# Kernel tuning notes

Hardware: AMD Instinct MI355X
Metric: run time of the kernel (lower is better)

## Reference

```python
import jax, jax.numpy as jnp
import numpy as np

B, S, H, A, I = 64, 512, 1024, 1024, 1024


def setup_inputs() -> dict:
    key = jax.random.key(0)
    ks = jax.random.split(key, 12)
    s = lambda fan_in: 1.0 / np.sqrt(fan_in)
    return {
        "encoded": jax.random.normal(ks[0], (B, S, H), jnp.float32),
        "inputs": jax.random.normal(ks[1], (B, I), jnp.float32),
        "states": jax.random.normal(ks[2], (B, H), jnp.float32),
        # attention params
        "W_enc": jax.random.uniform(ks[3], (H, A), jnp.float32, -s(H), s(H)),
        "b_enc": jnp.zeros((A,), jnp.float32),
        "W_dec": jax.random.uniform(ks[4], (H, A), jnp.float32, -s(H), s(H)),
        "b_dec": jnp.zeros((A,), jnp.float32),
        "w_out": jax.random.uniform(ks[5], (A, 1), jnp.float32, -s(A), s(A)),
        "b_out": jnp.zeros((1,), jnp.float32),
        # GRU cell params (input size = I + H)
        "W_ih": jax.random.uniform(ks[6], (3 * H, I + H), jnp.float32, -s(H), s(H)),
        "W_hh": jax.random.uniform(ks[7], (3 * H, H), jnp.float32, -s(H), s(H)),
        "b_ih": jax.random.uniform(ks[8], (3 * H,), jnp.float32, -s(H), s(H)),
        "b_hh": jax.random.uniform(ks[9], (3 * H,), jnp.float32, -s(H), s(H)),
    }


def reference(encoded, inputs, states, W_enc, b_enc, W_dec, b_dec, w_out, b_out,
              W_ih, W_hh, b_ih, b_hh):
    # setup_memory: project encoder states  [B,S,H] @ [H,A] -> [B,S,A]
    enc_proj = jnp.einsum("bsh,ha->bsa", encoded, W_enc) + b_enc
    # project decoder state and broadcast over S
    dec_proj = states @ W_dec + b_dec                      # [B,A]
    projected = enc_proj + dec_proj[:, None, :]            # [B,S,A]
    scores = jnp.tanh(projected) @ w_out + b_out           # [B,S,1]
    weights = jax.nn.softmax(scores, axis=1)               # [B,S,1]
    attention = jnp.sum(encoded * weights, axis=1)         # [B,H]
    # GRU cell on concatenated input
    x = jnp.concatenate([inputs, attention], axis=1)       # [B,I+H]
    gi = x @ W_ih.T + b_ih                                 # [B,3H]
    gh = states @ W_hh.T + b_hh                            # [B,3H]
    i_r, i_z, i_n = jnp.split(gi, 3, axis=1)
    h_r, h_z, h_n = jnp.split(gh, 3, axis=1)
    r = jax.nn.sigmoid(i_r + h_r)
    z = jax.nn.sigmoid(i_z + h_z)
    n = jnp.tanh(i_n + r * h_n)
    return (1.0 - z) * n + z * states                      # [B,H]
```

## Files before the change

### kernel.cpp

```cpp
#include <hip/hip_runtime.h>
#include <stdint.h>

typedef __bf16 bf16x8 __attribute__((ext_vector_type(8)));
typedef float f32x4 __attribute__((ext_vector_type(4)));
typedef unsigned short u16x8 __attribute__((ext_vector_type(8)));

#define LOG2E 1.4426950408889634f
#define LSTR 32

__device__ __forceinline__ unsigned short f2bf(float f) {
  unsigned int x = __builtin_bit_cast(unsigned int, f);
  x += 0x7FFFu + ((x >> 16) & 1u);
  return (unsigned short)(x >> 16);
}
__device__ __forceinline__ float bflo(unsigned int u) {
  return __builtin_bit_cast(float, u << 16);
}
__device__ __forceinline__ float bfhi(unsigned int u) {
  return __builtin_bit_cast(float, u & 0xffff0000u);
}
__device__ __forceinline__ float tanh_fast(float x) {
  float cx = fminf(fmaxf(x, -15.f), 15.f);
  float e = __builtin_amdgcn_exp2f(cx * (2.f * LOG2E));
  return (e - 1.f) * __builtin_amdgcn_rcpf(e + 1.f);
}
__device__ __forceinline__ float sigmoid_fast(float x) {
  float cx = fminf(fmaxf(x, -30.f), 30.f);
  float e = __builtin_amdgcn_exp2f(cx * LOG2E);
  return e * __builtin_amdgcn_rcpf(e + 1.f);
}
__device__ __forceinline__ ushort4 cvt4(const float4 f) {
  return make_ushort4(f2bf(f.x), f2bf(f.y), f2bf(f.z), f2bf(f.w));
}

__device__ __forceinline__ void gl_lds16(const unsigned short* g,
                                         const unsigned short* lds_base) {
  __builtin_amdgcn_global_load_lds(
      (const __attribute__((address_space(1))) unsigned int*)(uintptr_t)g,
      (__attribute__((address_space(3))) unsigned int*)(unsigned int)(uintptr_t)lds_base,
      16, 0, 0);
}

__global__ __launch_bounds__(256) void k_conv(const float* __restrict__ enc,
                                              unsigned short* __restrict__ encb) {
  const size_t base = ((size_t)blockIdx.x * 256) * 64 + (size_t)threadIdx.x * 8;
  float4 v[16];
#pragma unroll
  for (int c = 0; c < 8; ++c) {
    const size_t i = base + (size_t)c * 2048;
    v[2 * c]     = *(const float4*)(enc + i);
    v[2 * c + 1] = *(const float4*)(enc + i + 4);
  }
#pragma unroll
  for (int c = 0; c < 8; ++c) {
    const size_t i = base + (size_t)c * 2048;
    const ushort4 a = cvt4(v[2 * c]);
    const ushort4 b = cvt4(v[2 * c + 1]);
    u16x8 pk = {a.x, a.y, a.z, a.w, b.x, b.y, b.z, b.w};
    *(u16x8*)(encb + i) = pk;
  }
}

__global__ __launch_bounds__(256) void k_small(
    const float* __restrict__ W_enc, unsigned short* __restrict__ Wt,
    const float* __restrict__ states, const float* __restrict__ W_dec,
    const float* __restrict__ b_dec, const float* __restrict__ b_enc,
    float* __restrict__ dvec, float4* __restrict__ zbase) {
  __shared__ unsigned short tile[64][65];
  __shared__ float red[256];
  const int bid = blockIdx.x;
  const int tid = threadIdx.x;
  if (bid < 256) {
    const int bx = bid & 15, by = bid >> 4;
    const int x = tid & 63, y0 = tid >> 6;
#pragma unroll
    for (int i = y0; i < 64; i += 4)
      tile[i][x] = f2bf(W_enc[(size_t)(by * 64 + i) * 1024 + bx * 64 + x]);
    __syncthreads();
#pragma unroll
    for (int i = y0; i < 64; i += 4)
      Wt[(size_t)(bx * 64 + i) * 1024 + by * 64 + x] = tile[x][i];
  } else if (bid < 768) {
    const int bb = bid - 256;
    const int b = bb >> 3;
    const int a0 = (bb & 7) * 128;
    const int a = tid & 127, half = tid >> 7;
    const float* sp = states + (size_t)b * 1024;
    const float* wp = W_dec + a0 + a;
    float acc = 0.f;
    const int kb = half * 512;
#pragma unroll 8
    for (int k = kb; k < kb + 512; ++k)
      acc += sp[k] * wp[(size_t)k * 1024];
    red[tid] = acc;
    __syncthreads();
    if (tid < 128) {
      float v = red[tid] + red[tid + 128];
      dvec[(size_t)b * 1024 + a0 + tid] = v + b_dec[a0 + tid] + b_enc[a0 + tid];
    }
  } else {
    const float4 z = {0.f, 0.f, 0.f, 0.f};
    zbase[(size_t)(bid - 768) * 256 + tid] = z;
  }
}

__global__ __launch_bounds__(256, 3) void k_scores_bf16(
    const unsigned short* __restrict__ encb,
    const unsigned short* __restrict__ Wt,
    const float* __restrict__ dvec,
    const float* __restrict__ w_out,
    float* __restrict__ scores) {
  __shared__ alignas(16) unsigned short lds[2][8192];
  __shared__ float sc[128];

  const int tid = threadIdx.x;
  const int wave = tid >> 6, lane = tid & 63;
  const int l15 = lane & 15, quad = lane >> 4;
  const int mt = blockIdx.x >> 3;
  const int nt = blockIdx.x & 7;
  const int row0 = mt * 128;
  const int b = row0 >> 9;
  const int wm = (wave >> 1) * 64, wn = (wave & 1) * 64;
  const int srow = lane >> 2;
  const int fsw = ((lane >> 2) & 3) ^ ((lane >> 4) & 3);
  const int skoff = (((lane & 3) ^ fsw) * 8);
  const int rchunk = ((quad ^ ((l15 & 3) ^ ((l15 >> 2) & 3))) * 8);

  if (tid < 128) sc[tid] = 0.f;

  const unsigned short* gsrc[4];
#pragma unroll
  for (int s = 0; s < 4; ++s) {
    const int g = wave * 4 + s;
    gsrc[s] = (g < 8)
        ? encb + (size_t)(row0 + g * 16 + srow) * 1024 + skoff
        : Wt + (size_t)(nt * 128 + (g - 8) * 16 + srow) * 1024 + skoff;
  }

  const f32x4 vz = {0.f, 0.f, 0.f, 0.f};
  f32x4 acc[4][4];
#pragma unroll
  for (int i = 0; i < 4; ++i)
#pragma unroll
    for (int j = 0; j < 4; ++j) acc[i][j] = vz;

#define STAGE(BUF, KK)                                              \
  do {                                                              \
    _Pragma("unroll") for (int s = 0; s < 4; ++s)                   \
        gl_lds16(gsrc[s] + (KK), &lds[BUF][(wave * 4 + s) * 512]);  \
  } while (0)

#define COMPUTE(BUF)                                                          \
  do {                                                                        \
    bf16x8 af[4], bg[4];                                                      \
    _Pragma("unroll") for (int i = 0; i < 4; ++i)                             \
        af[i] = *(const bf16x8*)(&lds[BUF][(wm + i * 16 + l15) * LSTR + rchunk]); \
    _Pragma("unroll") for (int j = 0; j < 4; ++j)                             \
        bg[j] = *(const bf16x8*)(&lds[BUF][4096 + (wn + j * 16 + l15) * LSTR + rchunk]); \
    _Pragma("unroll") for (int i = 0; i < 4; ++i)                             \
      _Pragma("unroll") for (int j = 0; j < 4; ++j)                           \
          acc[i][j] = __builtin_amdgcn_mfma_f32_16x16x32_bf16(af[i], bg[j],   \
                                                              acc[i][j], 0, 0, 0); \
  } while (0)

  STAGE(0, 0);
  __syncthreads();

#pragma unroll 1
  for (int k0 = 0; k0 < 1024; k0 += 64) {
    STAGE(1, k0 + 32);
    COMPUTE(0);
    __syncthreads();
    if (k0 + 64 < 1024) { STAGE(0, k0 + 64); }
    COMPUTE(1);
    __syncthreads();
  }
#undef STAGE
#undef COMPUTE

  float p[4][4];
#pragma unroll
  for (int i = 0; i < 4; ++i)
#pragma unroll
    for (int r = 0; r < 4; ++r) p[i][r] = 0.f;
#pragma unroll
  for (int j = 0; j < 4; ++j) {
    const int a = nt * 128 + wn + j * 16 + l15;
    const float dv = dvec[(size_t)b * 1024 + a];
    const float wo = w_out[a];
#pragma unroll
    for (int i = 0; i < 4; ++i)
#pragma unroll
      for (int r = 0; r < 4; ++r)
        p[i][r] += tanh_fast(acc[i][j][r] + dv) * wo;
  }
#pragma unroll
  for (int i = 0; i < 4; ++i)
#pragma unroll
    for (int r = 0; r < 4; ++r) {
      float v = p[i][r];
      v += __shfl_xor(v, 1);
      v += __shfl_xor(v, 2);
      v += __shfl_xor(v, 4);
      v += __shfl_xor(v, 8);
      if (l15 == 0) atomicAdd(&sc[wm + i * 16 + quad * 4 + r], v);
    }
  __syncthreads();
  if (tid < 128)
    atomicAdd(&scores[(size_t)b * 512 + (row0 & 511) + tid], sc[tid]);
}

__global__ __launch_bounds__(256) void k_scores_f32(
    const float* __restrict__ enc, const unsigned short* __restrict__ Wt,
    const float* __restrict__ dvec, const float* __restrict__ w_out,
    float* __restrict__ scores) {
  __shared__ alignas(16) unsigned short lA[128 * LSTR];
  __shared__ alignas(16) unsigned short lB[128 * LSTR];
  __shared__ float sc[128];
  const int tid = threadIdx.x;
  const int wave = tid >> 6, lane = tid & 63;
  const int l15 = lane & 15, quad = lane >> 4;
  const int mt = blockIdx.x >> 2, nh = blockIdx.x & 3;
  const int row0 = mt * 128, b = row0 >> 9;
  const int wm = (wave >> 1) * 64, wn = (wave & 1) * 64;
  const int srow = lane >> 2, skoff = (lane & 3) * 8;
  if (tid < 128) sc[tid] = 0.f;
  const f32x4 vz = {0.f, 0.f, 0.f, 0.f};
#pragma unroll 1
  for (int t2 = 0; t2 < 2; ++t2) {
    const int nt = nh * 2 + t2;
    f32x4 acc[4][4];
#pragma unroll
    for (int i = 0; i < 4; ++i)
#pragma unroll
      for (int j = 0; j < 4; ++j) acc[i][j] = vz;
#pragma unroll 1
    for (int k0 = 0; k0 < 1024; k0 += 32) {
      ushort4 sa[2][2];
      uint4 vb[2];
#pragma unroll
      for (int rr = 0; rr < 2; ++rr) {
        const int r = wave * 2 + rr;
        const float* ap = enc + (size_t)(row0 + r * 16 + srow) * 1024 + k0 + skoff;
        sa[rr][0] = cvt4(*(const float4*)ap);
        sa[rr][1] = cvt4(*(const float4*)(ap + 4));
        vb[rr] = *(const uint4*)(Wt + (size_t)(nt * 128 + r * 16 + srow) * 1024 + k0 + skoff);
      }
      __syncthreads();
#pragma unroll
      for (int rr = 0; rr < 2; ++rr) {
        const int r = wave * 2 + rr;
        *(ushort4*)(lA + (r * 16 + srow) * LSTR + skoff) = sa[rr][0];
        *(ushort4*)(lA + (r * 16 + srow) * LSTR + skoff + 4) = sa[rr][1];
        *(uint4*)(lB + (r * 16 + srow) * LSTR + skoff) = vb[rr];
      }
      __syncthreads();
      bf16x8 af[4], bg[4];
#pragma unroll
      for (int i = 0; i < 4; ++i)
        af[i] = *(const bf16x8*)(lA + (wm + i * 16 + l15) * LSTR + quad * 8);
#pragma unroll
      for (int j = 0; j < 4; ++j)
        bg[j] = *(const bf16x8*)(lB + (wn + j * 16 + l15) * LSTR + quad * 8);
#pragma unroll
      for (int i = 0; i < 4; ++i)
#pragma unroll
        for (int j = 0; j < 4; ++j)
          acc[i][j] = __builtin_amdgcn_mfma_f32_16x16x32_bf16(af[i], bg[j],
                                                              acc[i][j], 0, 0, 0);
    }
    float p[4][4];
#pragma unroll
    for (int i = 0; i < 4; ++i)
#pragma unroll
      for (int r = 0; r < 4; ++r) p[i][r] = 0.f;
#pragma unroll
    for (int j = 0; j < 4; ++j) {
      const int a = nt * 128 + wn + j * 16 + l15;
      const float dv = dvec[(size_t)b * 1024 + a];
      const float wo = w_out[a];
#pragma unroll
      for (int i = 0; i < 4; ++i)
#pragma unroll
        for (int r = 0; r < 4; ++r)
          p[i][r] += tanh_fast(acc[i][j][r] + dv) * wo;
    }
#pragma unroll
    for (int i = 0; i < 4; ++i)
#pragma unroll
      for (int r = 0; r < 4; ++r) {
        float v = p[i][r];
        v += __shfl_xor(v, 1);
        v += __shfl_xor(v, 2);
        v += __shfl_xor(v, 4);
        v += __shfl_xor(v, 8);
        if (l15 == 0) atomicAdd(&sc[wm + i * 16 + quad * 4 + r], v);
      }
  }
  __syncthreads();
  if (tid < 128)
    atomicAdd(&scores[(size_t)b * 512 + (row0 & 511) + tid], sc[tid]);
}

template <bool ABF16>
__global__ __launch_bounds__(256) void k_attn(const void* __restrict__ encv,
                                              const float* __restrict__ scores,
                                              float* __restrict__ att) {
  const int b = blockIdx.x >> 2;
  const int scn = blockIdx.x & 3;
  const int tid = threadIdx.x;
  __shared__ float w[512];
  __shared__ float redm[4], reds[4];

  const float s0 = scores[(size_t)b * 512 + tid];
  const float s1 = scores[(size_t)b * 512 + 256 + tid];
  float m = fmaxf(s0, s1);
#pragma unroll
  for (int off = 32; off; off >>= 1) m = fmaxf(m, __shfl_xor(m, off));
  const int wv = tid >> 6;
  if ((tid & 63) == 0) redm[wv] = m;
  __syncthreads();
  m = fmaxf(fmaxf(redm[0], redm[1]), fmaxf(redm[2], redm[3]));
  const float e0 = __builtin_amdgcn_exp2f((s0 - m) * LOG2E);
  const float e1 = __builtin_amdgcn_exp2f((s1 - m) * LOG2E);
  float sum = e0 + e1;
#pragma unroll
  for (int off = 32; off; off >>= 1) sum += __shfl_xor(sum, off);
  if ((tid & 63) == 0) reds[wv] = sum;
  __syncthreads();
  sum = reds[0] + reds[1] + reds[2] + reds[3];
  const float inv = 1.f / sum;
  w[tid] = e0 * inv;
  w[tid + 256] = e1 * inv;
  __syncthreads();

  const int h0 = (tid & 127) * 8;
  const int sh = tid >> 7;
  float a[8];
#pragma unroll
  for (int i = 0; i < 8; ++i) a[i] = 0.f;
  const size_t base = ((size_t)(b * 512 + scn * 128 + sh)) * 1024 + h0;
#pragma unroll 4
  for (int i = 0; i < 64; ++i) {
    const float ws_ = w[scn * 128 + sh + 2 * i];
    if constexpr (ABF16) {
      const uint4 v = *(const uint4*)((const unsigned short*)encv + base + (size_t)(2 * i) * 1024);
      a[0] += ws_ * bflo(v.x); a[1] += ws_ * bfhi(v.x);
      a[2] += ws_ * bflo(v.y); a[3] += ws_ * bfhi(v.y);
      a[4] += ws_ * bflo(v.z); a[5] += ws_ * bfhi(v.z);
      a[6] += ws_ * bflo(v.w); a[7] += ws_ * bfhi(v.w);
    } else {
      const float* ep = (const float*)encv + base + (size_t)(2 * i) * 1024;
      const float4 v0 = *(const float4*)ep;
      const float4 v1 = *(const float4*)(ep + 4);
      a[0] += ws_ * v0.x; a[1] += ws_ * v0.y;
      a[2] += ws_ * v0.z; a[3] += ws_ * v0.w;
      a[4] += ws_ * v1.x; a[5] += ws_ * v1.y;
      a[6] += ws_ * v1.z; a[7] += ws_ * v1.w;
    }
  }
#pragma unroll
  for (int i = 0; i < 8; ++i)
    atomicAdd(&att[(size_t)b * 1024 + h0 + i], a[i]);
}

__global__ __launch_bounds__(256) void k_gru_gemm(
    const float* __restrict__ xin,
    const float* __restrict__ att,
    const float* __restrict__ states,
    const float* __restrict__ W_ih,
    const float* __restrict__ W_hh,
    float* __restrict__ gbuf) {
  const int tid = threadIdx.x;
  const int wave = tid >> 6, lane = tid & 63;
  const int l15 = lane & 15, quad = lane >> 4;
  const int kk = blockIdx.x & 3;
  const int rest = blockIdx.x >> 2;
  const bool is_gh = rest >= 48;
  const int nt = is_gh ? rest - 48 : rest;
  const int n0 = nt * 64;
  const int KT = is_gh ? 1024 : 2048;
  const int Kh = KT >> 2;
  const int kbase = kk * Kh;
  const float* W = is_gh ? W_hh : W_ih;
  float* outp = gbuf + (is_gh ? (size_t)64 * 3072 : 0);

  __shared__ alignas(16) unsigned short lA[64 * LSTR];
  __shared__ alignas(16) unsigned short lB[64 * LSTR];

  const f32x4 vz = {0.f, 0.f, 0.f, 0.f};
  f32x4 acc[2][2];
  acc[0][0] = vz; acc[0][1] = vz; acc[1][0] = vz; acc[1][1] = vz;

  const int arow = tid >> 2;
  const int achunk = (tid & 3) * 8;
  const int fswG = ((tid >> 2) & 3) ^ ((tid >> 4) & 3);
  const int wchunk = (((tid & 3) ^ fswG) * 8);
  const int rchunkG = ((quad ^ ((l15 & 3) ^ ((l15 >> 2) & 3))) * 8);
  const int wm2 = (wave >> 1) * 32, wn2 = (wave & 1) * 32;

  float4 ra0, ra1, rb0, rb1;
  auto LOADK = [&](int kg0) {
    const int kg = kg0 + achunk;
    const float* ap = is_gh ? (states + (size_t)arow * 1024 + kg)
                    : (kg < 1024 ? (xin + (size_t)arow * 1024 + kg)
                                 : (att + (size_t)arow * 1024 + (kg - 1024)));
    ra0 = *(const float4*)ap;
    ra1 = *(const float4*)(ap + 4);
    const float* wp = W + (size_t)(n0 + arow) * KT + kg;
    rb0 = *(const float4*)wp;
    rb1 = *(const float4*)(wp + 4);
  };
  LOADK(kbase);

#pragma unroll 1
  for (int k0 = 0; k0 < Kh; k0 += 32) {
    __syncthreads();
    *(ushort4*)(lA + arow * LSTR + wchunk) = cvt4(ra0);
    *(ushort4*)(lA + arow * LSTR + wchunk + 4) = cvt4(ra1);
    *(ushort4*)(lB + arow * LSTR + wchunk) = cvt4(rb0);
    *(ushort4*)(lB + arow * LSTR + wchunk + 4) = cvt4(rb1);
    __syncthreads();
    if (k0 + 32 < Kh) LOADK(kbase + k0 + 32);
    bf16x8 af[2], bg[2];
#pragma unroll
    for (int i = 0; i < 2; ++i)
      af[i] = *(const bf16x8*)(lA + (wm2 + i * 16 + l15) * LSTR + rchunkG);
#pragma unroll
    for (int j = 0; j < 2; ++j)
      bg[j] = *(const bf16x8*)(lB + (wn2 + j * 16 + l15) * LSTR + rchunkG);
#pragma unroll
    for (int i = 0; i < 2; ++i)
#pragma unroll
      for (int j = 0; j < 2; ++j)
        acc[i][j] = __builtin_amdgcn_mfma_f32_16x16x32_bf16(af[i], bg[j],
                                                            acc[i][j], 0, 0, 0);
  }
#pragma unroll
  for (int i = 0; i < 2; ++i)
#pragma unroll
    for (int j = 0; j < 2; ++j)
#pragma unroll
      for (int r = 0; r < 4; ++r) {
        const int m = wm2 + i * 16 + quad * 4 + r;
        const int n = n0 + wn2 + j * 16 + l15;
        atomicAdd(&outp[(size_t)m * 3072 + n], acc[i][j][r]);
      }
}

__global__ void k_gate(const float* __restrict__ gbuf,
                       const float* __restrict__ states,
                       const float* __restrict__ b_ih,
                       const float* __restrict__ b_hh,
                       float* __restrict__ outp) {
  const int idx = blockIdx.x * 256 + threadIdx.x;
  const int b = idx >> 10, h = idx & 1023;
  const float* gi = gbuf + (size_t)b * 3072;
  const float* gh = gbuf + (size_t)64 * 3072 + (size_t)b * 3072;
  const float ir = gi[h] + b_ih[h];
  const float iz = gi[1024 + h] + b_ih[1024 + h];
  const float in_ = gi[2048 + h] + b_ih[2048 + h];
  const float hr = gh[h] + b_hh[h];
  const float hz = gh[1024 + h] + b_hh[1024 + h];
  const float hn = gh[2048 + h] + b_hh[2048 + h];
  const float r = sigmoid_fast(ir + hr);
  const float z = sigmoid_fast(iz + hz);
  const float n = tanh_fast(in_ + r * hn);
  const float hp = states[idx];
  outp[idx] = (1.f - z) * n + z * hp;
}

extern "C" void kernel_launch(void* const* d_in, const int* in_sizes, int n_in,
                              void* d_out, int out_size, void* d_ws, size_t ws_size,
                              hipStream_t stream) {
  const float* enc    = (const float*)d_in[0];
  const float* xin    = (const float*)d_in[1];
  const float* states = (const float*)d_in[2];
  const float* W_enc  = (const float*)d_in[3];
  const float* b_enc  = (const float*)d_in[4];
  const float* W_dec  = (const float*)d_in[5];
  const float* b_dec  = (const float*)d_in[6];
  const float* w_out  = (const float*)d_in[7];
  const float* W_ih   = (const float*)d_in[9];
  const float* W_hh   = (const float*)d_in[10];
  const float* b_ih   = (const float*)d_in[11];
  const float* b_hh   = (const float*)d_in[12];
  float* out = (float*)d_out;

  const size_t ENC_BF16_BYTES = (size_t)32768 * 1024 * 2;
  const bool use_bf16 = ws_size >= ENC_BF16_BYTES + (8u << 20);

  char* ws = (char*)d_ws;
  unsigned short* encb = (unsigned short*)ws;
  char* base = ws + (use_bf16 ? ENC_BF16_BYTES : 0);
  unsigned short* Wt = (unsigned short*)base;
  float* dvec    = (float*)(base + 2097152);
  float* scoresb = (float*)(base + 2097152 + 262144);
  float* att     = (float*)(base + 2097152 + 262144 + 131072);
  float* gbuf    = (float*)(base + 2097152 + 262144 + 131072 + 262144);

  k_small<<<1248, 256, 0, stream>>>(W_enc, Wt, states, W_dec, b_dec, b_enc,
                                    dvec, (float4*)scoresb);
  if (use_bf16) {
    k_conv<<<2048, 256, 0, stream>>>(enc, encb);
    k_scores_bf16<<<2048, 256, 0, stream>>>(encb, Wt, dvec, w_out, scoresb);
    k_attn<true><<<256, 256, 0, stream>>>(encb, scoresb, att);
  } else {
    k_scores_f32<<<1024, 256, 0, stream>>>(enc, Wt, dvec, w_out, scoresb);
    k_attn<false><<<256, 256, 0, stream>>>(enc, scoresb, att);
  }
  k_gru_gemm<<<384, 256, 0, stream>>>(xin, att, states, W_ih, W_hh, gbuf);
  k_gate<<<256, 256, 0, stream>>>(gbuf, states, b_ih, b_hh, out);
}
```

Measured before the change: 435.9 us.

## Fuse conversion into prep kernel, triple-buffer scores GEMM, split attention, prefetch GRU loads

Folds the fp32-to-bf16 conversion of the encoder into the prep kernel to save a launch. The scores GEMM moves from a double-buffered loop with two barriers per step to a three-stage LDS ring with explicit vmcnt waits, one barrier per step and raised priority around the MFMA block. The attention kernel splits the sequence into 8 chunks instead of 4, doubling its grid. The GRU GEMM issues the next global loads before the barrier into separate registers so they overlap the LDS stores. The extra LDS buffer may reduce occupancy, and the hand-written wait counts must match the outstanding loads exactly.

```diff
diff --git a/kernel.cpp b/kernel.cpp
--- a/kernel.cpp
+++ b/kernel.cpp
@@ -41,31 +41,12 @@
       16, 0, 0);
 }
 
-__global__ __launch_bounds__(256) void k_conv(const float* __restrict__ enc,
-                                              unsigned short* __restrict__ encb) {
-  const size_t base = ((size_t)blockIdx.x * 256) * 64 + (size_t)threadIdx.x * 8;
-  float4 v[16];
-#pragma unroll
-  for (int c = 0; c < 8; ++c) {
-    const size_t i = base + (size_t)c * 2048;
-    v[2 * c]     = *(const float4*)(enc + i);
-    v[2 * c + 1] = *(const float4*)(enc + i + 4);
-  }
-#pragma unroll
-  for (int c = 0; c < 8; ++c) {
-    const size_t i = base + (size_t)c * 2048;
-    const ushort4 a = cvt4(v[2 * c]);
-    const ushort4 b = cvt4(v[2 * c + 1]);
-    u16x8 pk = {a.x, a.y, a.z, a.w, b.x, b.y, b.z, b.w};
-    *(u16x8*)(encb + i) = pk;
-  }
-}
-
-__global__ __launch_bounds__(256) void k_small(
+__global__ __launch_bounds__(256) void k_prep(
     const float* __restrict__ W_enc, unsigned short* __restrict__ Wt,
     const float* __restrict__ states, const float* __restrict__ W_dec,
     const float* __restrict__ b_dec, const float* __restrict__ b_enc,
-    float* __restrict__ dvec, float4* __restrict__ zbase) {
+    float* __restrict__ dvec, float4* __restrict__ zbase,
+    const float* __restrict__ enc, unsigned short* __restrict__ encb) {
   __shared__ unsigned short tile[64][65];
   __shared__ float red[256];
   const int bid = blockIdx.x;
@@ -98,9 +79,26 @@
       float v = red[tid] + red[tid + 128];
       dvec[(size_t)b * 1024 + a0 + tid] = v + b_dec[a0 + tid] + b_enc[a0 + tid];
     }
-  } else {
+  } else if (bid < 1248) {
     const float4 z = {0.f, 0.f, 0.f, 0.f};
     zbase[(size_t)(bid - 768) * 256 + tid] = z;
+  } else {
+    const size_t base = ((size_t)(bid - 1248) * 256) * 64 + (size_t)tid * 8;
+    float4 v[16];
+#pragma unroll
+    for (int c = 0; c < 8; ++c) {
+      const size_t i = base + (size_t)c * 2048;
+      v[2 * c]     = *(const float4*)(enc + i);
+      v[2 * c + 1] = *(const float4*)(enc + i + 4);
+    }
+#pragma unroll
+    for (int c = 0; c < 8; ++c) {
+      const size_t i = base + (size_t)c * 2048;
+      const ushort4 a = cvt4(v[2 * c]);
+      const ushort4 b = cvt4(v[2 * c + 1]);
+      u16x8 pk = {a.x, a.y, a.z, a.w, b.x, b.y, b.z, b.w};
+      *(u16x8*)(encb + i) = pk;
+    }
   }
 }
 
@@ -110,7 +108,7 @@
     const float* __restrict__ dvec,
     const float* __restrict__ w_out,
     float* __restrict__ scores) {
-  __shared__ alignas(16) unsigned short lds[2][8192];
+  __shared__ alignas(16) unsigned short lds[3][8192];
   __shared__ float sc[128];
 
   const int tid = threadIdx.x;
@@ -144,39 +142,53 @@
 #pragma unroll
     for (int j = 0; j < 4; ++j) acc[i][j] = vz;
 
-#define STAGE(BUF, KK)                                              \
-  do {                                                              \
-    _Pragma("unroll") for (int s = 0; s < 4; ++s)                   \
-        gl_lds16(gsrc[s] + (KK), &lds[BUF][(wave * 4 + s) * 512]);  \
-  } while (0)
-
-#define COMPUTE(BUF)                                                          \
-  do {                                                                        \
-    bf16x8 af[4], bg[4];                                                      \
-    _Pragma("unroll") for (int i = 0; i < 4; ++i)                             \
-        af[i] = *(const bf16x8*)(&lds[BUF][(wm + i * 16 + l15) * LSTR + rchunk]); \
-    _Pragma("unroll") for (int j = 0; j < 4; ++j)                             \
-        bg[j] = *(const bf16x8*)(&lds[BUF][4096 + (wn + j * 16 + l15) * LSTR + rchunk]); \
-    _Pragma("unroll") for (int i = 0; i < 4; ++i)                             \
-      _Pragma("unroll") for (int j = 0; j < 4; ++j)                           \
-          acc[i][j] = __builtin_amdgcn_mfma_f32_16x16x32_bf16(af[i], bg[j],   \
-                                                              acc[i][j], 0, 0, 0); \
-  } while (0)
+  auto STAGE = [&](int bi, int kk) {
+    unsigned short* base = &lds[0][0] + bi * 8192;
+#pragma unroll
+    for (int s = 0; s < 4; ++s)
+      gl_lds16(gsrc[s] + kk, base + (wave * 4 + s) * 512);
+  };
+  auto COMPUTE = [&](int bi) {
+    const unsigned short* base = &lds[0][0] + bi * 8192;
+    bf16x8 af[4], bg[4];
+#pragma unroll
+    for (int i = 0; i < 4; ++i)
+      af[i] = *(const bf16x8*)(base + (wm + i * 16 + l15) * LSTR + rchunk);
+#pragma unroll
+    for (int j = 0; j < 4; ++j)
+      bg[j] = *(const bf16x8*)(base + 4096 + (wn + j * 16 + l15) * LSTR + rchunk);
+    __builtin_amdgcn_s_setprio(1);
+#pragma unroll
+    for (int i = 0; i < 4; ++i)
+#pragma unroll
+      for (int j = 0; j < 4; ++j)
+        acc[i][j] = __builtin_amdgcn_mfma_f32_16x16x32_bf16(af[i], bg[j],
+                                                            acc[i][j], 0, 0, 0);
+    __builtin_amdgcn_s_setprio(0);
+  };
 
   STAGE(0, 0);
-  __syncthreads();
-
+  STAGE(1, 32);
+  int cur = 0;
 #pragma unroll 1
-  for (int k0 = 0; k0 < 1024; k0 += 64) {
-    STAGE(1, k0 + 32);
-    COMPUTE(0);
-    __syncthreads();
-    if (k0 + 64 < 1024) { STAGE(0, k0 + 64); }
-    COMPUTE(1);
-    __syncthreads();
-  }
-#undef STAGE
-#undef COMPUTE
+  for (int t = 0; t < 30; ++t) {
+    asm volatile("s_waitcnt vmcnt(4)" ::: "memory");
+    __builtin_amdgcn_s_barrier();
+    __builtin_amdgcn_sched_barrier(0);
+    int stg = cur + 2; if (stg >= 3) stg -= 3;
+    STAGE(stg, (t + 2) * 32);
+    COMPUTE(cur);
+    cur = (cur == 2) ? 0 : cur + 1;
+  }
+  asm volatile("s_waitcnt vmcnt(4)" ::: "memory");
+  __builtin_amdgcn_s_barrier();
+  __builtin_amdgcn_sched_barrier(0);
+  COMPUTE(cur);
+  cur = (cur == 2) ? 0 : cur + 1;
+  asm volatile("s_waitcnt vmcnt(0)" ::: "memory");
+  __builtin_amdgcn_s_barrier();
+  __builtin_amdgcn_sched_barrier(0);
+  COMPUTE(cur);
 
   float p[4][4];
 #pragma unroll
@@ -306,8 +318,8 @@
 __global__ __launch_bounds__(256) void k_attn(const void* __restrict__ encv,
                                               const float* __restrict__ scores,
                                               float* __restrict__ att) {
-  const int b = blockIdx.x >> 2;
-  const int scn = blockIdx.x & 3;
+  const int b = blockIdx.x >> 3;
+  const int scn = blockIdx.x & 7;
   const int tid = threadIdx.x;
   __shared__ float w[512];
   __shared__ float redm[4], reds[4];
@@ -339,10 +351,10 @@
   float a[8];
 #pragma unroll
   for (int i = 0; i < 8; ++i) a[i] = 0.f;
-  const size_t base = ((size_t)(b * 512 + scn * 128 + sh)) * 1024 + h0;
-#pragma unroll 4
-  for (int i = 0; i < 64; ++i) {
-    const float ws_ = w[scn * 128 + sh + 2 * i];
+  const size_t base = ((size_t)(b * 512 + scn * 64 + sh)) * 1024 + h0;
+#pragma unroll 8
+  for (int i = 0; i < 32; ++i) {
+    const float ws_ = w[scn * 64 + sh + 2 * i];
     if constexpr (ABF16) {
       const uint4 v = *(const uint4*)((const unsigned short*)encv + base + (size_t)(2 * i) * 1024);
       a[0] += ws_ * bflo(v.x); a[1] += ws_ * bfhi(v.x);
@@ -399,29 +411,29 @@
   const int rchunkG = ((quad ^ ((l15 & 3) ^ ((l15 >> 2) & 3))) * 8);
   const int wm2 = (wave >> 1) * 32, wn2 = (wave & 1) * 32;
 
-  float4 ra0, ra1, rb0, rb1;
-  auto LOADK = [&](int kg0) {
+  float4 ca0, ca1, cb0, cb1, na0, na1, nb0, nb1;
+  auto LOADK = [&](int kg0, float4& a0, float4& a1, float4& b0, float4& b1) {
     const int kg = kg0 + achunk;
     const float* ap = is_gh ? (states + (size_t)arow * 1024 + kg)
                     : (kg < 1024 ? (xin + (size_t)arow * 1024 + kg)
                                  : (att + (size_t)arow * 1024 + (kg - 1024)));
-    ra0 = *(const float4*)ap;
-    ra1 = *(const float4*)(ap + 4);
+    a0 = *(const float4*)ap;
+    a1 = *(const float4*)(ap + 4);
     const float* wp = W + (size_t)(n0 + arow) * KT + kg;
-    rb0 = *(const float4*)wp;
-    rb1 = *(const float4*)(wp + 4);
+    b0 = *(const float4*)wp;
+    b1 = *(const float4*)(wp + 4);
   };
-  LOADK(kbase);
+  LOADK(kbase, ca0, ca1, cb0, cb1);
 
 #pragma unroll 1
   for (int k0 = 0; k0 < Kh; k0 += 32) {
+    if (k0 + 32 < Kh) LOADK(kbase + k0 + 32, na0, na1, nb0, nb1);
     __syncthreads();
-    *(ushort4*)(lA + arow * LSTR + wchunk) = cvt4(ra0);
-    *(ushort4*)(lA + arow * LSTR + wchunk + 4) = cvt4(ra1);
-    *(ushort4*)(lB + arow * LSTR + wchunk) = cvt4(rb0);
-    *(ushort4*)(lB + arow * LSTR + wchunk + 4) = cvt4(rb1);
+    *(ushort4*)(lA + arow * LSTR + wchunk) = cvt4(ca0);
+    *(ushort4*)(lA + arow * LSTR + wchunk + 4) = cvt4(ca1);
+    *(ushort4*)(lB + arow * LSTR + wchunk) = cvt4(cb0);
+    *(ushort4*)(lB + arow * LSTR + wchunk + 4) = cvt4(cb1);
     __syncthreads();
-    if (k0 + 32 < Kh) LOADK(kbase + k0 + 32);
     bf16x8 af[2], bg[2];
 #pragma unroll
     for (int i = 0; i < 2; ++i)
@@ -435,6 +447,7 @@
       for (int j = 0; j < 2; ++j)
         acc[i][j] = __builtin_amdgcn_mfma_f32_16x16x32_bf16(af[i], bg[j],
                                                             acc[i][j], 0, 0, 0);
+    ca0 = na0; ca1 = na1; cb0 = nb0; cb1 = nb1;
   }
 #pragma unroll
   for (int i = 0; i < 2; ++i)
@@ -499,15 +512,15 @@
   float* att     = (float*)(base + 2097152 + 262144 + 131072);
   float* gbuf    = (float*)(base + 2097152 + 262144 + 131072 + 262144);
 
-  k_small<<<1248, 256, 0, stream>>>(W_enc, Wt, states, W_dec, b_dec, b_enc,
-                                    dvec, (float4*)scoresb);
+  const int prep_grid = use_bf16 ? 3296 : 1248;
+  k_prep<<<prep_grid, 256, 0, stream>>>(W_enc, Wt, states, W_dec, b_dec, b_enc,
+                                        dvec, (float4*)scoresb, enc, encb);
   if (use_bf16) {
-    k_conv<<<2048, 256, 0, stream>>>(enc, encb);
     k_scores_bf16<<<2048, 256, 0, stream>>>(encb, Wt, dvec, w_out, scoresb);
-    k_attn<true><<<256, 256, 0, stream>>>(encb, scoresb, att);
+    k_attn<true><<<512, 256, 0, stream>>>(encb, scoresb, att);
   } else {
     k_scores_f32<<<1024, 256, 0, stream>>>(enc, Wt, dvec, w_out, scoresb);
-    k_attn<false><<<256, 256, 0, stream>>>(enc, scoresb, att);
+    k_attn<false><<<512, 256, 0, stream>>>(enc, scoresb, att);
   }
   k_gru_gemm<<<384, 256, 0, stream>>>(xin, att, states, W_ih, W_hh, gbuf);
   k_gate<<<256, 256, 0, stream>>>(gbuf, states, b_ih, b_hh, out);
```

Result: no change. 433.0 us (-0.7%).
